# Performance work log

Hardware: AMD Instinct MI355X
Metric: run time of the kernel (lower is better)

## Reference

```python
import jax, jax.numpy as jnp
import numpy as np

B, S, E, H = 4, 1024, 1024, 16

def setup_inputs() -> dict:
    key = jax.random.key(0)
    ks = jax.random.split(key, 7)
    sc = 0.02
    return {
        "queries": jax.random.normal(ks[0], (B, S, E), jnp.float32),
        "keys": jax.random.normal(ks[1], (B, S, E), jnp.float32),
        "values": jax.random.normal(ks[2], (B, S, E), jnp.float32),
        "Wq_w": jax.random.normal(ks[3], (E, E), jnp.float32) * sc,
        "Wq_b": jax.random.normal(ks[4], (E,), jnp.float32) * sc,
        "Wo_w": jax.random.normal(ks[5], (E, E), jnp.float32) * sc,
        "Wo_b": jax.random.normal(ks[6], (E,), jnp.float32) * sc,
        "num_heads": H,
    }

def reference(queries, keys, values, Wq_w, Wq_b, Wo_w, Wo_b, num_heads):
    b, s, e = queries.shape
    dh = e // num_heads

    def proj_heads(x):
        # NOTE: original module applies Wq to q, k AND v (bug kept faithfully)
        y = x @ Wq_w.T + Wq_b                      # [b, s, e]
        return y.reshape(b, s, num_heads, dh)      # [b, s, h, dh]

    q = proj_heads(queries)
    k = proj_heads(keys)
    v = proj_heads(values)

    scores = jnp.einsum('bqhd,bkhd->bhqk', q, k) / jnp.sqrt(jnp.asarray(dh, q.dtype))
    attn = jax.nn.softmax(scores, axis=-1)         # [b, h, q, k]
    out = jnp.einsum('bhqk,bkhd->bqhd', attn, v)   # [b, s, h, dh]
    out = out.reshape(b, s, e)
    return out @ Wo_w.T + Wo_b
```

## Files before the change

### kernel.cpp

```cpp
#include <hip/hip_runtime.h>
#include <stdint.h>


typedef __attribute__((ext_vector_type(8))) short bf16x8;
typedef __attribute__((ext_vector_type(4))) float f32x4;
typedef __attribute__((ext_vector_type(4))) short short4v;

#define GLOAD_LDS(gp, lp)                                                      \
  __builtin_amdgcn_global_load_lds(                                            \
      (__attribute__((address_space(1))) void*)(gp),                           \
      (__attribute__((address_space(3))) void*)(lp), 16, 0, 0)

__device__ __forceinline__ unsigned short f2bf(float f) {
  union { float f; unsigned u; } v; v.f = f;
  unsigned r = v.u + 0x7FFFu + ((v.u >> 16) & 1u);
  return (unsigned short)(r >> 16);
}

template<int CTRL>
__device__ __forceinline__ float dpp_rr(float x) {
  union { float f; int i; } a, r;
  a.f = x;
  r.i = __builtin_amdgcn_update_dpp(0, a.i, CTRL, 0xf, 0xf, false);
  return r.f;
}
__device__ __forceinline__ float rowmax16(float x) {
  x = fmaxf(x, dpp_rr<0x121>(x));
  x = fmaxf(x, dpp_rr<0x122>(x));
  x = fmaxf(x, dpp_rr<0x124>(x));
  x = fmaxf(x, dpp_rr<0x128>(x));
  return x;
}
__device__ __forceinline__ float rowsum16(float x) {
  x += dpp_rr<0x121>(x);
  x += dpp_rr<0x122>(x);
  x += dpp_rr<0x124>(x);
  x += dpp_rr<0x128>(x);
  return x;
}

__global__ void cvt_all(const float* __restrict__ q, const float* __restrict__ k,
                        const float* __restrict__ v, const float* __restrict__ wq,
                        const float* __restrict__ wo, short* __restrict__ dst) {
  int i = blockIdx.x * 256 + threadIdx.x;
  const float* src; int j;
  if (i < 1048576)      { src = q;  j = i; }
  else if (i < 2097152) { src = k;  j = i - 1048576; }
  else if (i < 3145728) { src = v;  j = i - 2097152; }
  else if (i < 3407872) { src = wq; j = i - 3145728; }
  else                  { src = wo; j = i - 3407872; }
  float4 f = reinterpret_cast<const float4*>(src)[j];
  short4v o;
  o.x = (short)f2bf(f.x); o.y = (short)f2bf(f.y);
  o.z = (short)f2bf(f.z); o.w = (short)f2bf(f.w);
  reinterpret_cast<short4v*>(dst)[i] = o;
}

template<int EPI>
__global__ __launch_bounds__(256, 2)
void gemm_bt(const short* __restrict__ A, const short* __restrict__ Bw,
             const float* __restrict__ bias,
             short* __restrict__ qkv, float* __restrict__ outf)
{
  __shared__ short As[128 * 64];
  __shared__ short Bs[128 * 64];
  const int tid  = threadIdx.x;
  const int lane = tid & 63;
  const int g    = lane >> 4;
  const int r7   = lane & 7;
  const int w    = tid >> 6;
  const int wm   = w >> 1, wn = w & 1;

  const int orig = blockIdx.y * 8 + blockIdx.x;
  const int cpx  = (gridDim.x * gridDim.y) >> 3;
  const int t    = (orig & 7) * cpx + (orig >> 3);
  const int m0   = (t >> 3) * 128, n0 = (t & 7) * 128;

  f32x4 acc[4][4] = {};

  for (int k0 = 0; k0 < 1024; k0 += 64) {
#pragma unroll
    for (int c = 0; c < 4; c++) {
      int L   = c * 256 + tid;
      int row = L >> 3;
      int col = ((L & 7) ^ (row & 7)) * 8;
      GLOAD_LDS(A  + (m0 + row) * 1024 + k0 + col, As + L * 8);
      GLOAD_LDS(Bw + (n0 + row) * 1024 + k0 + col, Bs + L * 8);
    }
    __syncthreads();
#pragma unroll
    for (int kk = 0; kk < 2; kk++) {
      bf16x8 av[4], bv[4];
#pragma unroll
      for (int mi = 0; mi < 4; mi++) {
        int row = wm * 64 + mi * 16 + (lane & 15);
        av[mi] = *(const bf16x8*)&As[row * 64 + (((kk * 4 + g) ^ r7) * 8)];
      }
#pragma unroll
      for (int ni = 0; ni < 4; ni++) {
        int row = wn * 64 + ni * 16 + (lane & 15);
        bv[ni] = *(const bf16x8*)&Bs[row * 64 + (((kk * 4 + g) ^ r7) * 8)];
      }
#pragma unroll
      for (int mi = 0; mi < 4; mi++)
#pragma unroll
        for (int ni = 0; ni < 4; ni++)
          acc[mi][ni] = __builtin_amdgcn_mfma_f32_16x16x32_bf16(av[mi], bv[ni], acc[mi][ni], 0, 0, 0);
    }
    __syncthreads();
  }

  if (EPI == 0) {
    const int inp = m0 >> 12;
#pragma unroll
    for (int mi = 0; mi < 4; mi++) {
#pragma unroll
      for (int ni = 0; ni < 4; ni++) {
        const int coll = n0 + wn * 64 + ni * 16 + (lane & 15);
        const float bv = bias[coll];
        const int rbase = m0 + wm * 64 + mi * 16 + (lane >> 4) * 4;
        const int hh = coll >> 6, d = coll & 63;
        if (inp < 2) {
#pragma unroll
          for (int j = 0; j < 4; j++) {
            int rowl = rbase + j;
            int bb = (rowl >> 10) & 3, s = rowl & 1023;
            qkv[(((inp * 4 + bb) * 16 + hh) * 1024 + s) * 64 + d] =
                (short)f2bf(acc[mi][ni][j] + bv);
          }
        } else {
          int bb = (rbase >> 10) & 3, s0 = rbase & 1023;
          short4v o;
          o.x = (short)f2bf(acc[mi][ni][0] + bv);
          o.y = (short)f2bf(acc[mi][ni][1] + bv);
          o.z = (short)f2bf(acc[mi][ni][2] + bv);
          o.w = (short)f2bf(acc[mi][ni][3] + bv);
          *(short4v*)&qkv[8 * 1024 * 1024 + ((bb * 16 + hh) * 64 + d) * 1024 + s0] = o;
        }
      }
    }
  } else {
#pragma unroll
    for (int mi = 0; mi < 4; mi++) {
#pragma unroll
      for (int ni = 0; ni < 4; ni++) {
        const int coll = n0 + wn * 64 + ni * 16 + (lane & 15);
        const float bv = bias[coll];
        const int rbase = m0 + wm * 64 + mi * 16 + (lane >> 4) * 4;
#pragma unroll
        for (int j = 0; j < 4; j++)
          outf[(rbase + j) * 1024 + coll] = acc[mi][ni][j] + bv;
      }
    }
  }
}

__global__ __launch_bounds__(256, 2)
void attn_kernel(const short* __restrict__ qkv, short* __restrict__ O)
{
  __shared__ short Ks[2][64 * 64];
  __shared__ short VTs[2][64 * 64];
  __shared__ short QPs[64 * 64];

  const int tid  = threadIdx.x;
  const int lane = tid & 63;
  const int g    = lane >> 4, r7 = lane & 7;
  const int w    = tid >> 6;

  const int t   = (blockIdx.x & 7) * 128 + (blockIdx.x >> 3);
  const int qt  = t & 15, hh = (t >> 4) & 15, bb = t >> 8;
  const int q0  = qt * 64;

  const short* Qg = qkv + (bb * 16 + hh) * 1024 * 64;
  const short* Kg = qkv + 4 * 1024 * 1024 + (bb * 16 + hh) * 1024 * 64;
  const short* Vg = qkv + 8 * 1024 * 1024 + (bb * 16 + hh) * 64 * 1024;

#pragma unroll
  for (int c = 0; c < 2; c++) {
    int L = c * 256 + tid;
    int row = L >> 3;
    int col = ((L & 7) ^ (row & 7)) * 8;
    GLOAD_LDS(Qg + (q0 + row) * 64 + col, QPs + L * 8);
    GLOAD_LDS(Kg + row * 64 + col,        &Ks[0][L * 8]);
    GLOAD_LDS(Vg + row * 1024 + col,      &VTs[0][L * 8]);
  }
  __syncthreads();
  bf16x8 qf[2];
  {
    const int qrow = w * 16 + (lane & 15);
    qf[0] = *(const bf16x8*)&QPs[qrow * 64 + ((g ^ r7) * 8)];
    qf[1] = *(const bf16x8*)&QPs[qrow * 64 + (((4 + g) ^ r7) * 8)];
  }

  const float SC = 0.125f * 1.44269504f;
  float m_run[4], l_run[4];
  f32x4 acc_o[4] = {};
#pragma unroll
  for (int j = 0; j < 4; j++) { m_run[j] = -1e30f; l_run[j] = 0.0f; }

  int cur = 0;
  for (int kt = 0; kt < 16; kt++) {
    if (kt < 15) {
#pragma unroll
      for (int c = 0; c < 2; c++) {
        int L = c * 256 + tid;
        int row = L >> 3;
        int col = ((L & 7) ^ (row & 7)) * 8;
        GLOAD_LDS(Kg + ((kt + 1) * 64 + row) * 64 + col, &Ks[cur ^ 1][L * 8]);
        GLOAD_LDS(Vg + row * 1024 + (kt + 1) * 64 + col, &VTs[cur ^ 1][L * 8]);
      }
    }

    f32x4 sa[4] = {};
#pragma unroll
    for (int kk = 0; kk < 2; kk++) {
#pragma unroll
      for (int ni = 0; ni < 4; ni++) {
        int krow = ni * 16 + (lane & 15);
        bf16x8 kf = *(const bf16x8*)&Ks[cur][krow * 64 + (((kk * 4 + g) ^ r7) * 8)];
        sa[ni] = __builtin_amdgcn_mfma_f32_16x16x32_bf16(qf[kk], kf, sa[ni], 0, 0, 0);
      }
    }
    float mt[4], alpha[4], rs[4];
#pragma unroll
    for (int j = 0; j < 4; j++) {
      mt[j] = rowmax16(fmaxf(fmaxf(sa[0][j], sa[1][j]), fmaxf(sa[2][j], sa[3][j])));
      float mn = fmaxf(m_run[j], mt[j] * SC);
      alpha[j] = __builtin_amdgcn_exp2f(m_run[j] - mn);
      m_run[j] = mn;
      rs[j] = 0.0f;
    }
#pragma unroll
    for (int ni = 0; ni < 4; ni++) {
      int col = ni * 16 + (lane & 15);
#pragma unroll
      for (int j = 0; j < 4; j++) {
        int row = w * 16 + g * 4 + j;
        float p = __builtin_amdgcn_exp2f(sa[ni][j] * SC - m_run[j]);
        rs[j] += p;
        QPs[row * 64 + (col ^ ((row & 7) << 3))] = (short)f2bf(p);
      }
    }
#pragma unroll
    for (int j = 0; j < 4; j++) {
      rs[j] = rowsum16(rs[j]);
      l_run[j] = l_run[j] * alpha[j] + rs[j];
    }
#pragma unroll
    for (int di = 0; di < 4; di++)
#pragma unroll
      for (int j = 0; j < 4; j++)
        acc_o[di][j] *= alpha[j];
#pragma unroll
    for (int kk = 0; kk < 2; kk++) {
      int prow = w * 16 + (lane & 15);
      bf16x8 pf = *(const bf16x8*)&QPs[prow * 64 + (((kk * 4 + g) ^ r7) * 8)];
#pragma unroll
      for (int di = 0; di < 4; di++) {
        int vrow = di * 16 + (lane & 15);
        bf16x8 vf = *(const bf16x8*)&VTs[cur][vrow * 64 + (((kk * 4 + g) ^ r7) * 8)];
        acc_o[di] = __builtin_amdgcn_mfma_f32_16x16x32_bf16(pf, vf, acc_o[di], 0, 0, 0);
      }
    }
    __syncthreads();
    cur ^= 1;
  }

#pragma unroll
  for (int di = 0; di < 4; di++) {
    int d = hh * 64 + di * 16 + (lane & 15);
#pragma unroll
    for (int j = 0; j < 4; j++) {
      int q = q0 + w * 16 + g * 4 + j;
      O[(bb * 1024 + q) * 1024 + d] = (short)f2bf(acc_o[di][j] / l_run[j]);
    }
  }
}

extern "C" void kernel_launch(void* const* d_in, const int* in_sizes, int n_in,
                              void* d_out, int out_size, void* d_ws, size_t ws_size,
                              hipStream_t stream)
{
  (void)in_sizes; (void)n_in; (void)out_size; (void)ws_size;
  const float* q    = (const float*)d_in[0];
  const float* k    = (const float*)d_in[1];
  const float* v    = (const float*)d_in[2];
  const float* Wq_w = (const float*)d_in[3];
  const float* Wq_b = (const float*)d_in[4];
  const float* Wo_w = (const float*)d_in[5];
  const float* Wo_b = (const float*)d_in[6];
  float* out = (float*)d_out;

  short* ws   = (short*)d_ws;
  short* Xbf  = ws;
  short* Obf  = ws;
  short* Wqb  = ws + 12582912;
  short* Wob  = ws + 13631488;
  short* qkv  = ws + 14680064;

  cvt_all<<<14336, 256, 0, stream>>>(q, k, v, Wq_w, Wo_w, ws);

  dim3 gp(8, 96);
  gemm_bt<0><<<gp, 256, 0, stream>>>(Xbf, Wqb, Wq_b, qkv, nullptr);

  attn_kernel<<<1024, 256, 0, stream>>>(qkv, Obf);

  dim3 gf(8, 32);
  gemm_bt<1><<<gf, 256, 0, stream>>>(Obf, Wob, Wo_b, nullptr, out);
}
```

Measured before the change: 206.5 us.

## Lazy softmax rescale, MFMA row-sum, fast bf16 rounding, setprio in attention

The attention inner loop now rescales the running max and accumulators only when some row's new max exceeds the old one by more than a threshold, chosen wave-wide with __any. The softmax denominator is no longer built with DPP reductions and is instead accumulated by an extra MFMA against a ones vector, read at the end with a shuffle. P conversion uses a cheaper round-half-up bf16 conversion, and s_setprio raises priority around the MFMA sections. These cut VALU and DPP work per tile at the cost of one extra MFMA per kk step and slightly different rounding, with a bounded risk of overflow from the lazy max.

```diff
diff --git a/kernel.cpp b/kernel.cpp
--- a/kernel.cpp
+++ b/kernel.cpp
@@ -15,6 +15,10 @@
   union { float f; unsigned u; } v; v.f = f;
   unsigned r = v.u + 0x7FFFu + ((v.u >> 16) & 1u);
   return (unsigned short)(r >> 16);
+}
+__device__ __forceinline__ unsigned short f2bf_fast(float f) {
+  union { float f; unsigned u; } v; v.f = f;
+  return (unsigned short)((v.u + 0x8000u) >> 16);
 }
 
 template<int CTRL>
@@ -29,13 +33,6 @@
   x = fmaxf(x, dpp_rr<0x122>(x));
   x = fmaxf(x, dpp_rr<0x124>(x));
   x = fmaxf(x, dpp_rr<0x128>(x));
-  return x;
-}
-__device__ __forceinline__ float rowsum16(float x) {
-  x += dpp_rr<0x121>(x);
-  x += dpp_rr<0x122>(x);
-  x += dpp_rr<0x124>(x);
-  x += dpp_rr<0x128>(x);
   return x;
 }
 
@@ -164,6 +161,7 @@
 
   const int tid  = threadIdx.x;
   const int lane = tid & 63;
+  const int l15  = lane & 15;
   const int g    = lane >> 4, r7 = lane & 7;
   const int w    = tid >> 6;
 
@@ -187,16 +185,22 @@
   __syncthreads();
   bf16x8 qf[2];
   {
-    const int qrow = w * 16 + (lane & 15);
+    const int qrow = w * 16 + l15;
     qf[0] = *(const bf16x8*)&QPs[qrow * 64 + ((g ^ r7) * 8)];
     qf[1] = *(const bf16x8*)&QPs[qrow * 64 + (((4 + g) ^ r7) * 8)];
   }
+  bf16x8 vf_l = {};
+  if (l15 == 0) {
+#pragma unroll
+    for (int x = 0; x < 8; x++) vf_l[x] = (short)0x3F80;
+  }
 
   const float SC = 0.125f * 1.44269504f;
-  float m_run[4], l_run[4];
+  float m_run[4];
+  f32x4 acc_l = {};
   f32x4 acc_o[4] = {};
 #pragma unroll
-  for (int j = 0; j < 4; j++) { m_run[j] = -1e30f; l_run[j] = 0.0f; }
+  for (int j = 0; j < 4; j++) m_run[j] = -1e30f;
 
   int cur = 0;
   for (int kt = 0; kt < 16; kt++) {
@@ -212,67 +216,78 @@
     }
 
     f32x4 sa[4] = {};
+    __builtin_amdgcn_s_setprio(1);
 #pragma unroll
     for (int kk = 0; kk < 2; kk++) {
 #pragma unroll
       for (int ni = 0; ni < 4; ni++) {
-        int krow = ni * 16 + (lane & 15);
+        int krow = ni * 16 + l15;
         bf16x8 kf = *(const bf16x8*)&Ks[cur][krow * 64 + (((kk * 4 + g) ^ r7) * 8)];
         sa[ni] = __builtin_amdgcn_mfma_f32_16x16x32_bf16(qf[kk], kf, sa[ni], 0, 0, 0);
       }
     }
-    float mt[4], alpha[4], rs[4];
-#pragma unroll
-    for (int j = 0; j < 4; j++) {
-      mt[j] = rowmax16(fmaxf(fmaxf(sa[0][j], sa[1][j]), fmaxf(sa[2][j], sa[3][j])));
-      float mn = fmaxf(m_run[j], mt[j] * SC);
-      alpha[j] = __builtin_amdgcn_exp2f(m_run[j] - mn);
-      m_run[j] = mn;
-      rs[j] = 0.0f;
+    __builtin_amdgcn_s_setprio(0);
+
+    float mtl[4];
+#pragma unroll
+    for (int j = 0; j < 4; j++)
+      mtl[j] = fmaxf(fmaxf(sa[0][j], sa[1][j]), fmaxf(sa[2][j], sa[3][j])) * SC;
+    float nd = fmaxf(fmaxf(mtl[0] - m_run[0], mtl[1] - m_run[1]),
+                     fmaxf(mtl[2] - m_run[2], mtl[3] - m_run[3]));
+    if (__any(nd > 8.0f)) {
+#pragma unroll
+      for (int j = 0; j < 4; j++) {
+        float mt = rowmax16(mtl[j]);
+        float mn = fmaxf(m_run[j], mt);
+        float alpha = __builtin_amdgcn_exp2f(m_run[j] - mn);
+        m_run[j] = mn;
+        acc_l[j] *= alpha;
+#pragma unroll
+        for (int di = 0; di < 4; di++) acc_o[di][j] *= alpha;
+      }
     }
 #pragma unroll
     for (int ni = 0; ni < 4; ni++) {
-      int col = ni * 16 + (lane & 15);
+      int col = ni * 16 + l15;
 #pragma unroll
       for (int j = 0; j < 4; j++) {
         int row = w * 16 + g * 4 + j;
         float p = __builtin_amdgcn_exp2f(sa[ni][j] * SC - m_run[j]);
-        rs[j] += p;
-        QPs[row * 64 + (col ^ ((row & 7) << 3))] = (short)f2bf(p);
-      }
-    }
-#pragma unroll
-    for (int j = 0; j < 4; j++) {
-      rs[j] = rowsum16(rs[j]);
-      l_run[j] = l_run[j] * alpha[j] + rs[j];
-    }
-#pragma unroll
-    for (int di = 0; di < 4; di++)
-#pragma unroll
-      for (int j = 0; j < 4; j++)
-        acc_o[di][j] *= alpha[j];
+        QPs[row * 64 + (col ^ ((row & 7) << 3))] = (short)f2bf_fast(p);
+      }
+    }
+    __builtin_amdgcn_s_setprio(1);
 #pragma unroll
     for (int kk = 0; kk < 2; kk++) {
-      int prow = w * 16 + (lane & 15);
+      int prow = w * 16 + l15;
       bf16x8 pf = *(const bf16x8*)&QPs[prow * 64 + (((kk * 4 + g) ^ r7) * 8)];
+      acc_l = __builtin_amdgcn_mfma_f32_16x16x32_bf16(pf, vf_l, acc_l, 0, 0, 0);
 #pragma unroll
       for (int di = 0; di < 4; di++) {
-        int vrow = di * 16 + (lane & 15);
+        int vrow = di * 16 + l15;
         bf16x8 vf = *(const bf16x8*)&VTs[cur][vrow * 64 + (((kk * 4 + g) ^ r7) * 8)];
         acc_o[di] = __builtin_amdgcn_mfma_f32_16x16x32_bf16(pf, vf, acc_o[di], 0, 0, 0);
       }
     }
+    __builtin_amdgcn_s_setprio(0);
     __syncthreads();
     cur ^= 1;
   }
 
+  float linv[4];
+#pragma unroll
+  for (int j = 0; j < 4; j++) {
+    float lv = __shfl(acc_l[j], lane & 48);
+    linv[j] = 1.0f / lv;
+  }
+
 #pragma unroll
   for (int di = 0; di < 4; di++) {
-    int d = hh * 64 + di * 16 + (lane & 15);
+    int d = hh * 64 + di * 16 + l15;
 #pragma unroll
     for (int j = 0; j < 4; j++) {
       int q = q0 + w * 16 + g * 4 + j;
-      O[(bb * 1024 + q) * 1024 + d] = (short)f2bf(acc_o[di][j] / l_run[j]);
+      O[(bb * 1024 + q) * 1024 + d] = (short)f2bf(acc_o[di][j] * linv[j]);
     }
   }
 }
```

Measured after the change: 190.4 us. -7.8%, faster.
